# Optimization experiments

Measured on AMD Instinct MI355X. Metric: run time of the kernel, lower is better.

Reference implementation:

```python
import jax, jax.numpy as jnp
import numpy as np
from math import sqrt

NUM_G = 32
N_HEADS = 8
D_MODEL = 512


def _linear(x, w, b):
    # torch nn.Linear: y = x @ W^T + b, W: (out, in)
    return jnp.einsum('...i,oi->...o', x, w) + b


def _full_attention(q, k, v):
    # q,k,v: [N, L, H, E]; no mask (mask_flag=False), dropout = identity (eval)
    E = q.shape[-1]
    scores = jnp.einsum('blhe,bshe->bhls', q, k)
    A = jax.nn.softmax(scores / sqrt(E), axis=-1)
    return jnp.einsum('bhls,bshd->blhd', A, v)


def setup_inputs() -> dict:
    key = jax.random.key(0)
    ks = jax.random.split(key, 15)
    B, ch, num_p, dim = 8, 1024, 8, D_MODEL
    x = jax.random.normal(ks[0], (B, ch, num_p, dim), dtype=jnp.float32)
    def lin(kw, kb):
        w = jax.random.normal(kw, (dim, dim), dtype=jnp.float32) * 0.02
        b = jax.random.normal(kb, (dim,), dtype=jnp.float32) * 0.02
        return w, b
    q1_w, q1_b = lin(ks[1], ks[2])
    k1_w, k1_b = lin(ks[3], ks[4])
    v1_w, v1_b = lin(ks[5], ks[6])
    q2_w, q2_b = lin(ks[7], ks[8])
    k2_w, k2_b = lin(ks[9], ks[10])
    v2_w, v2_b = lin(ks[11], ks[12])
    out_w, out_b = lin(ks[13], ks[14])
    return dict(x=x, q1_w=q1_w, q1_b=q1_b, k1_w=k1_w, k1_b=k1_b, v1_w=v1_w, v1_b=v1_b,
                q2_w=q2_w, q2_b=q2_b, k2_w=k2_w, k2_b=k2_b, v2_w=v2_w, v2_b=v2_b,
                out_w=out_w, out_b=out_b)


def reference(x, q1_w, q1_b, k1_w, k1_b, v1_w, v1_b,
              q2_w, q2_b, k2_w, k2_b, v2_w, v2_b, out_w, out_b):
    B, ch, num_p, dim = x.shape
    H, E = N_HEADS, dim // N_HEADS
    g = ch // NUM_G

    # 'B (num_g g) num_p p -> (B num_g num_p) g p'
    x1 = x.reshape(B, NUM_G, g, num_p, dim).transpose(0, 1, 3, 2, 4)
    x1 = x1.reshape(B * NUM_G * num_p, g, dim)

    # stage 1: inner-group attention over g
    q = _linear(x1, q1_w, q1_b).reshape(-1, g, H, E)
    k = _linear(x1, k1_w, k1_b).reshape(-1, g, H, E)
    v = _linear(x1, v1_w, v1_b).reshape(-1, g, H, E)
    y = _full_attention(q, k, v)  # [(B ng np), g, H, E]

    # '(B num_g num_p) g num_h p -> (B g num_p) num_g (num_h p)'
    y = y.reshape(B, NUM_G, num_p, g, H, E).transpose(0, 3, 2, 1, 4, 5)
    x2 = y.reshape(B * g * num_p, NUM_G, dim)

    # stage 2: inter-group attention over num_g
    q = _linear(x2, q2_w, q2_b).reshape(-1, NUM_G, H, E)
    k = _linear(x2, k2_w, k2_b).reshape(-1, NUM_G, H, E)
    v = _linear(x2, v2_w, v2_b).reshape(-1, NUM_G, H, E)
    y = _full_attention(q, k, v)  # [(B g np), num_g, H, E]

    # '(B g num_p) num_g num_h p -> B (num_g g) num_p (num_h p)'
    y = y.reshape(B, g, num_p, NUM_G, H, E).transpose(0, 3, 1, 2, 4, 5)
    y = y.reshape(B, ch, num_p, dim)

    return _linear(y, out_w, out_b)
```

## Files before the change

kernel.cpp:

```cpp
#include <hip/hip_runtime.h>
#include <hip/hip_bf16.h>

typedef __hip_bfloat16 bf16;
typedef __attribute__((ext_vector_type(8))) __bf16 bf16x8;
typedef __attribute__((ext_vector_type(4))) float f32x4;

__device__ __forceinline__ f32x4 mfma16(bf16x8 a, bf16x8 b, f32x4 c) {
  return __builtin_amdgcn_mfma_f32_16x16x32_bf16(a, b, c, 0, 0, 0);
}

__device__ __forceinline__ void gload_lds16(const void* g, void* lds) {
  __builtin_amdgcn_global_load_lds(
      (const __attribute__((address_space(1))) unsigned int*)g,
      (__attribute__((address_space(3))) unsigned int*)lds, 16, 0, 0);
}

__global__ __launch_bounds__(256)
void cvt_x_k(const float* __restrict__ s, bf16* __restrict__ d)
{
  const int i = (blockIdx.x * 256 + threadIdx.x) * 8;
  float4 a = *(const float4*)(s + i);
  float4 b = *(const float4*)(s + i + 4);
  union { bf16 h[8]; bf16x8 v; } u;
  u.h[0] = __float2bfloat16(a.x); u.h[1] = __float2bfloat16(a.y);
  u.h[2] = __float2bfloat16(a.z); u.h[3] = __float2bfloat16(a.w);
  u.h[4] = __float2bfloat16(b.x); u.h[5] = __float2bfloat16(b.y);
  u.h[6] = __float2bfloat16(b.z); u.h[7] = __float2bfloat16(b.w);
  *(bf16x8*)(d + i) = u.v;
}

__global__ __launch_bounds__(256)
void cvt_w_k(const float* s0, const float* s1, const float* s2, const float* s3,
             const float* s4, const float* s5, const float* s6, bf16* __restrict__ d)
{
  const int mat = blockIdx.x >> 7, blk = blockIdx.x & 127;
  const float* s;
  switch (mat) {
    case 0: s = s0; break; case 1: s = s1; break; case 2: s = s2; break;
    case 3: s = s3; break; case 4: s = s4; break; case 5: s = s5; break;
    default: s = s6; break;
  }
  const int i = (blk * 256 + threadIdx.x) * 8;
  float4 a = *(const float4*)(s + i);
  float4 b = *(const float4*)(s + i + 4);
  union { bf16 h[8]; bf16x8 v; } u;
  u.h[0] = __float2bfloat16(a.x); u.h[1] = __float2bfloat16(a.y);
  u.h[2] = __float2bfloat16(a.z); u.h[3] = __float2bfloat16(a.w);
  u.h[4] = __float2bfloat16(b.x); u.h[5] = __float2bfloat16(b.y);
  u.h[6] = __float2bfloat16(b.z); u.h[7] = __float2bfloat16(b.w);
  *(bf16x8*)(d + mat * 262144 + i) = u.v;
}

template<int MODE, int NBN>
__global__ __launch_bounds__(512)
void gemm2_k(const bf16* __restrict__ A,
             const bf16* __restrict__ W0, const bf16* __restrict__ W1, const bf16* __restrict__ W2,
             const float* __restrict__ Bi0, const float* __restrict__ Bi1, const float* __restrict__ Bi2,
             bf16* __restrict__ O0, bf16* __restrict__ O1, bf16* __restrict__ O2,
             float* __restrict__ F0)
{
  __shared__ __align__(16) char smem[131072];

  const int tid  = threadIdx.x;
  const int lane = tid & 63;
  const int wid  = tid >> 6;
  const int wm   = wid >> 2;
  const int wn   = wid & 3;
  const int lq   = lane & 15, qd = lane >> 4;

  const int per = gridDim.x >> 3;
  const int logical = (blockIdx.x & 7) * per + (blockIdx.x >> 3);
  const int bm = logical / NBN;
  const int bn = logical % NBN;
  const int m0 = bm * 256;
  const int n0 = bn * 256;

  const bf16* Wb; const float* Bsel; int nbase;
  if (MODE == 0) { Wb = W0; Bsel = Bi0; nbase = n0; }
  else {
    const int mat = n0 >> 9; nbase = n0 & 511;
    Wb   = (mat == 0) ? W0 : ((mat == 1) ? W1 : W2);
    Bsel = (mat == 0) ? Bi0 : ((mat == 1) ? Bi1 : Bi2);
  }

  f32x4 acc[8][4];
#pragma unroll
  for (int i = 0; i < 8; ++i)
#pragma unroll
    for (int j = 0; j < 4; ++j) acc[i][j] = f32x4{0.f, 0.f, 0.f, 0.f};

  auto stage_half = [&](int X, int h, int ktt, int tb) {
#pragma unroll
    for (int jj = 0; jj < 2; ++jj) {
      const int id = wid * 2 + jj;
      const int r  = id * 8 + (lane >> 3);
      const int cb = ktt * 128 + (((lane & 7) ^ (r & 7)) << 4);
      const char* g = X ? (const char*)Wb + (size_t)(nbase + h * 128 + r) * 1024 + cb
                        : (const char*)A  + (size_t)(m0   + h * 128 + r) * 1024 + cb;
      gload_lds16(g, smem + tb * 65536 + X * 32768 + h * 16384 + id * 1024);
    }
  };

  auto lda = [&](bf16x8 (&af)[4][2], const char* Ah) {
#pragma unroll
    for (int i = 0; i < 4; ++i) {
      const int row = wm * 64 + i * 16 + lq;
#pragma unroll
      for (int kk = 0; kk < 2; ++kk)
        af[i][kk] = *(const bf16x8*)(Ah + row * 128 + (((kk * 4 + qd) ^ (row & 7)) << 4));
    }
  };
  auto ldb = [&](bf16x8 (&bv)[2][2], const char* Bh) {
#pragma unroll
    for (int j = 0; j < 2; ++j) {
      const int row = wn * 32 + j * 16 + lq;
#pragma unroll
      for (int kk = 0; kk < 2; ++kk)
        bv[j][kk] = *(const bf16x8*)(Bh + row * 128 + (((kk * 4 + qd) ^ (row & 7)) << 4));
    }
  };

#define FMA_Q(AF, BV, QM, QN) do {                                               \
    __builtin_amdgcn_s_setprio(1);                                              \
    _Pragma("unroll") for (int kk = 0; kk < 2; ++kk)                             \
      _Pragma("unroll") for (int i = 0; i < 4; ++i)                              \
        _Pragma("unroll") for (int j = 0; j < 2; ++j)                            \
          acc[(QM) * 4 + i][(QN) * 2 + j] =                                      \
              mfma16(AF[i][kk], BV[j][kk], acc[(QM) * 4 + i][(QN) * 2 + j]);     \
    __builtin_amdgcn_s_setprio(0);                                               \
  } while (0)

#define PHASE_END() do {                                                         \
    asm volatile("s_waitcnt vmcnt(4)" ::: "memory");                             \
    __builtin_amdgcn_s_barrier();                                                \
    __builtin_amdgcn_sched_barrier(0);                                           \
  } while (0)

  stage_half(0, 0, 0, 0); stage_half(1, 0, 0, 0);
  stage_half(1, 1, 0, 0); stage_half(0, 1, 0, 0);
  stage_half(0, 0, 1, 1); stage_half(1, 1, 1, 1);
  PHASE_END();

  bf16x8 afA[4][2], afB[4][2], bv0[2][2], bv1[2][2];

  for (int kt = 0; kt < 8; ++kt) {
    const int bb = (kt & 1) * 65536;
    lda(afA, smem + bb);
    ldb(bv0, smem + bb + 32768);
    stage_half(0, 1, (kt + 1) & 7, (kt + 1) & 1);
    FMA_Q(afA, bv0, 0, 0);
    PHASE_END();
    ldb(bv1, smem + bb + 32768 + 16384);
    stage_half(1, 0, (kt + 1) & 7, (kt + 1) & 1);
    FMA_Q(afA, bv1, 0, 1);
    PHASE_END();
    lda(afB, smem + bb + 16384);
    stage_half(0, 0, (kt + 2) & 7, (kt + 2) & 1);
    FMA_Q(afB, bv1, 1, 1);
    PHASE_END();
    stage_half(1, 1, (kt + 2) & 7, (kt + 2) & 1);
    FMA_Q(afB, bv0, 1, 0);
    PHASE_END();
  }
#undef FMA_Q
#undef PHASE_END

  asm volatile("s_waitcnt vmcnt(0)" ::: "memory");
  __builtin_amdgcn_s_barrier();
  __builtin_amdgcn_sched_barrier(0);

  float biasv[4];
#pragma unroll
  for (int ni = 0; ni < 4; ++ni) {
    const int col = (ni >> 1) * 128 + wn * 32 + (ni & 1) * 16 + lq;
    biasv[ni] = Bsel[(MODE == 0) ? (n0 + col) : (nbase + col)];
  }

  if (MODE == 0) {
#pragma unroll
    for (int mi = 0; mi < 8; ++mi)
#pragma unroll
      for (int r = 0; r < 4; ++r) {
        const int m = m0 + (mi >> 2) * 128 + wm * 64 + (mi & 3) * 16 + qd * 4 + r;
#pragma unroll
        for (int ni = 0; ni < 4; ++ni) {
          const int n = n0 + (ni >> 1) * 128 + wn * 32 + (ni & 1) * 16 + lq;
          F0[(size_t)m * 512 + n] = acc[mi][ni][r] + biasv[ni];
        }
      }
  } else {
    const int mat = n0 >> 9;
    bf16* const Om = (mat == 0) ? O0 : ((mat == 1) ? O1 : O2);
    const int h0 = (n0 & 511) >> 6;
#pragma unroll
    for (int qm = 0; qm < 2; ++qm) {
#pragma unroll
      for (int i = 0; i < 4; ++i)
#pragma unroll
        for (int r = 0; r < 4; ++r) {
          const int row = wm * 64 + i * 16 + qd * 4 + r;
          const int sw  = (row & 7) ^ (((row >> 3) & 3) << 3);
#pragma unroll
          for (int ni = 0; ni < 4; ++ni) {
            const int col  = (ni >> 1) * 128 + wn * 32 + (ni & 1) * 16 + lq;
            const int byte = row * 512 + (((col >> 3) ^ sw) << 4) + (col & 7) * 2;
            *(bf16*)(smem + byte) = __float2bfloat16(acc[qm * 4 + i][ni][r] + biasv[ni]);
          }
        }
      __syncthreads();
      {
        const int hh   = tid >> 7;
        const int mrow = tid & 127;
        const int m    = m0 + qm * 128 + mrow;
        int a, seq;
        if (MODE == 1) {
          const int b = m >> 13, c = (m >> 3) & 1023, pp = m & 7;
          a = (b * 32 + (c >> 5)) * 8 + pp;  seq = c & 31;
        } else {
          a = m >> 5;  seq = m & 31;
        }
        const int sw = (mrow & 7) ^ (((mrow >> 3) & 3) << 3);
        bf16* const dst = Om + ((size_t)((a * 8 + h0 + hh) * 32 + seq)) * 64;
#pragma unroll
        for (int j = 0; j < 8; ++j) {
          const bf16x8 v = *(const bf16x8*)(smem + mrow * 512 + (((hh * 8 + j) ^ sw) << 4));
          *(bf16x8*)(dst + j * 8) = v;
        }
      }
      __syncthreads();
    }
  }
}

template<int STAGE>
__global__ __launch_bounds__(256)
void attn_k(const bf16* __restrict__ Q, const bf16* __restrict__ K,
            const bf16* __restrict__ V, bf16* __restrict__ Y)
{
  __shared__ __align__(16) char Plds[4][32 * 80];
  __shared__ __align__(16) char Vlds[4][32 * 132];
  const int tid  = threadIdx.x;
  const int lane = tid & 63;
  const int w    = tid >> 6;
  const int task = blockIdx.x * 4 + w;
  const int a = task >> 3, h = task & 7;
  const int lq = lane & 15, qd = lane >> 4;

  const bf16* Qb = Q + (size_t)(a * 8 + h) * 2048;
  const bf16* Kb = K + (size_t)(a * 8 + h) * 2048;
  const bf16* Vb = V + (size_t)(a * 8 + h) * 2048;

  {
    const int r  = lane >> 1;
    const int c0 = (lane & 1) * 32;
    union { bf16x8 v; unsigned u[4]; } t0, t1, t2, t3;
    t0.v = *(const bf16x8*)(Vb + r * 64 + c0);
    t1.v = *(const bf16x8*)(Vb + r * 64 + c0 + 8);
    t2.v = *(const bf16x8*)(Vb + r * 64 + c0 + 16);
    t3.v = *(const bf16x8*)(Vb + r * 64 + c0 + 24);
    unsigned* dst = (unsigned*)(Vlds[w] + r * 132 + c0 * 2);
#pragma unroll
    for (int j = 0; j < 4; ++j) dst[j]      = t0.u[j];
#pragma unroll
    for (int j = 0; j < 4; ++j) dst[4 + j]  = t1.u[j];
#pragma unroll
    for (int j = 0; j < 4; ++j) dst[8 + j]  = t2.u[j];
#pragma unroll
    for (int j = 0; j < 4; ++j) dst[12 + j] = t3.u[j];
  }

  bf16x8 qf[2][2], kf[2][2];
#pragma unroll
  for (int mi = 0; mi < 2; ++mi)
#pragma unroll
    for (int ks = 0; ks < 2; ++ks) {
      qf[mi][ks] = *(const bf16x8*)(Qb + (mi * 16 + lq) * 64 + ks * 32 + qd * 8);
      kf[mi][ks] = *(const bf16x8*)(Kb + (mi * 16 + lq) * 64 + ks * 32 + qd * 8);
    }

  f32x4 s[2][2];
#pragma unroll
  for (int mi = 0; mi < 2; ++mi)
#pragma unroll
    for (int ni = 0; ni < 2; ++ni) {
      s[mi][ni] = f32x4{0.f, 0.f, 0.f, 0.f};
#pragma unroll
      for (int ks = 0; ks < 2; ++ks)
        s[mi][ni] = mfma16(qf[mi][ks], kf[ni][ks], s[mi][ni]);
    }

  char* Pw = Plds[w];
  float rden[2][4];
#pragma unroll
  for (int mi = 0; mi < 2; ++mi) {
#pragma unroll
    for (int r = 0; r < 4; ++r) {
      float v0 = s[mi][0][r] * 0.125f, v1 = s[mi][1][r] * 0.125f;
      float mx = fmaxf(v0, v1);
#pragma unroll
      for (int d = 1; d < 16; d <<= 1) mx = fmaxf(mx, __shfl_xor(mx, d, 64));
      const float p0 = __expf(v0 - mx), p1 = __expf(v1 - mx);
      float sm = p0 + p1;
#pragma unroll
      for (int d = 1; d < 16; d <<= 1) sm += __shfl_xor(sm, d, 64);
      rden[mi][r] = 1.f / sm;
      const int qrow = mi * 16 + qd * 4 + r;
      bf16* prow = (bf16*)(Pw + qrow * 80);
      prow[lq]      = __float2bfloat16(p0);
      prow[16 + lq] = __float2bfloat16(p1);
    }
  }
  asm volatile("s_waitcnt lgkmcnt(0)" ::: "memory");
  __builtin_amdgcn_sched_barrier(0);

  bf16x8 pf[2];
#pragma unroll
  for (int mi = 0; mi < 2; ++mi)
    pf[mi] = *(const bf16x8*)(Pw + (mi * 16 + lq) * 80 + qd * 16);

  bf16x8 vf[4];
#pragma unroll
  for (int ni = 0; ni < 4; ++ni) {
    union { bf16 h[8]; bf16x8 v; } uv;
#pragma unroll
    for (int j = 0; j < 8; ++j)
      uv.h[j] = *(const bf16*)(Vlds[w] + (qd * 8 + j) * 132 + (ni * 16 + lq) * 2);
    vf[ni] = uv.v;
  }

  f32x4 o[2][4];
#pragma unroll
  for (int mi = 0; mi < 2; ++mi)
#pragma unroll
    for (int ni = 0; ni < 4; ++ni) {
      o[mi][ni] = f32x4{0.f, 0.f, 0.f, 0.f};
      o[mi][ni] = mfma16(pf[mi], vf[ni], o[mi][ni]);
    }

  int rowbase;
  if (STAGE == 1) { const int p = a & 7, ng = (a >> 3) & 31, b = a >> 8; rowbase = b * 8192 + p * 32 + ng; }
  else            { const int p = a & 7, i  = (a >> 3) & 31, b = a >> 8; rowbase = b * 8192 + i * 8 + p; }

#pragma unroll
  for (int mi = 0; mi < 2; ++mi) {
#pragma unroll
    for (int r = 0; r < 4; ++r) {
      const int q   = mi * 16 + qd * 4 + r;
      const int row = rowbase + q * 256;
      const float rd = rden[mi][r];
#pragma unroll
      for (int ni = 0; ni < 4; ++ni) {
        const int e = ni * 16 + lq;
        Y[(size_t)row * 512 + h * 64 + e] = __float2bfloat16(o[mi][ni][r] * rd);
      }
    }
  }
}

extern "C" void kernel_launch(void* const* d_in, const int* in_sizes, int n_in,
                              void* d_out, int out_size, void* d_ws, size_t ws_size,
                              hipStream_t stream) {
  const float* x   = (const float*)d_in[0];
  const float* q1w = (const float*)d_in[1];
  const float* q1b = (const float*)d_in[2];
  const float* k1w = (const float*)d_in[3];
  const float* k1b = (const float*)d_in[4];
  const float* v1w = (const float*)d_in[5];
  const float* v1b = (const float*)d_in[6];
  const float* q2w = (const float*)d_in[7];
  const float* q2b = (const float*)d_in[8];
  const float* k2w = (const float*)d_in[9];
  const float* k2b = (const float*)d_in[10];
  const float* v2w = (const float*)d_in[11];
  const float* v2b = (const float*)d_in[12];
  const float* ow  = (const float*)d_in[13];
  const float* ob  = (const float*)d_in[14];
  float* out = (float*)d_out;

  const size_t TOK = 65536ull * 512ull;
  const size_t WS1 = 262144;
  bf16* Xbf = (bf16*)d_ws;
  bf16* Qb  = Xbf + TOK;
  bf16* Kb  = Qb + TOK;
  bf16* Vb  = Kb + TOK;
  bf16* Wbf = Vb + TOK;
  bf16* X2  = Xbf;

  cvt_x_k<<<16384, 256, 0, stream>>>(x, Xbf);
  cvt_w_k<<<7 * 128, 256, 0, stream>>>(q1w, k1w, v1w, q2w, k2w, v2w, ow, Wbf);

  gemm2_k<1, 6><<<1536, 512, 0, stream>>>(Xbf, Wbf, Wbf + WS1, Wbf + 2 * WS1,
                                          q1b, k1b, v1b, Qb, Kb, Vb, nullptr);
  attn_k<1><<<4096, 256, 0, stream>>>(Qb, Kb, Vb, X2);
  gemm2_k<2, 6><<<1536, 512, 0, stream>>>(X2, Wbf + 3 * WS1, Wbf + 4 * WS1, Wbf + 5 * WS1,
                                          q2b, k2b, v2b, Qb, Kb, Vb, nullptr);
  attn_k<2><<<4096, 256, 0, stream>>>(Qb, Kb, Vb, X2);
  gemm2_k<0, 2><<<512, 512, 0, stream>>>(X2, Wbf + 6 * WS1, Wbf + 6 * WS1, Wbf + 6 * WS1,
                                         ob, ob, ob, nullptr, nullptr, nullptr, out);
}
```

Measured before the change: 501.2 us.

## Restructure GEMM prefetch to stage a full k-tile ahead per iteration

The GEMM main loop moves from per-phase vmcnt waits with staggered half-tile prefetches to a schedule that prefetches the whole k+2 tile into the buffer just consumed. The vmcnt wait now happens only at the end of each k-tile, and the inner phases keep plain barriers. The prologue stages two full tiles. This is meant to give global loads more time in flight and cut wait stalls, at the cost of a deeper prefetch and a buffer-reuse order that must stay race-free.

```diff
diff --git a/kernel.cpp b/kernel.cpp
--- a/kernel.cpp
+++ b/kernel.cpp
@@ -130,40 +130,49 @@
     __builtin_amdgcn_s_setprio(0);                                               \
   } while (0)
 
-#define PHASE_END() do {                                                         \
-    asm volatile("s_waitcnt vmcnt(4)" ::: "memory");                             \
+#define PHASE_BAR() do {                                                         \
     __builtin_amdgcn_s_barrier();                                                \
     __builtin_amdgcn_sched_barrier(0);                                           \
   } while (0)
 
+#define KTILE_END() do {                                                         \
+    asm volatile("s_waitcnt vmcnt(8)" ::: "memory");                             \
+    __builtin_amdgcn_s_barrier();                                                \
+    __builtin_amdgcn_sched_barrier(0);                                           \
+  } while (0)
+
   stage_half(0, 0, 0, 0); stage_half(1, 0, 0, 0);
   stage_half(1, 1, 0, 0); stage_half(0, 1, 0, 0);
-  stage_half(0, 0, 1, 1); stage_half(1, 1, 1, 1);
-  PHASE_END();
+  stage_half(0, 0, 1, 1); stage_half(1, 0, 1, 1);
+  stage_half(1, 1, 1, 1); stage_half(0, 1, 1, 1);
+  KTILE_END();
 
   bf16x8 afA[4][2], afB[4][2], bv0[2][2], bv1[2][2];
 
   for (int kt = 0; kt < 8; ++kt) {
     const int bb = (kt & 1) * 65536;
+    const int k2 = (kt + 2) & 7;
+    const int tb = kt & 1;
     lda(afA, smem + bb);
     ldb(bv0, smem + bb + 32768);
-    stage_half(0, 1, (kt + 1) & 7, (kt + 1) & 1);
     FMA_Q(afA, bv0, 0, 0);
-    PHASE_END();
+    PHASE_BAR();
     ldb(bv1, smem + bb + 32768 + 16384);
-    stage_half(1, 0, (kt + 1) & 7, (kt + 1) & 1);
+    stage_half(0, 0, k2, tb);
+    stage_half(1, 0, k2, tb);
     FMA_Q(afA, bv1, 0, 1);
-    PHASE_END();
+    PHASE_BAR();
     lda(afB, smem + bb + 16384);
-    stage_half(0, 0, (kt + 2) & 7, (kt + 2) & 1);
+    stage_half(1, 1, k2, tb);
     FMA_Q(afB, bv1, 1, 1);
-    PHASE_END();
-    stage_half(1, 1, (kt + 2) & 7, (kt + 2) & 1);
+    PHASE_BAR();
+    stage_half(0, 1, k2, tb);
     FMA_Q(afB, bv0, 1, 0);
-    PHASE_END();
+    KTILE_END();
   }
 #undef FMA_Q
-#undef PHASE_END
+#undef PHASE_BAR
+#undef KTILE_END
 
   asm volatile("s_waitcnt vmcnt(0)" ::: "memory");
   __builtin_amdgcn_s_barrier();
```

Measured after the change: 499.4 us. No clear change (-0.4%).
